# Performance work log

Hardware: AMD Instinct MI355X
Metric: run time of the kernel (lower is better)

The kernel has to match this reference:

```python
import jax, jax.numpy as jnp
import numpy as np

G, D, F, B, T = 8, 20, 160, 64, 2000  # groups, dims(hidden), feature=G*D, batch, time


def _lstm_layer(x, Wih, Whh, bih, bhh):
    # x: [B, T, Din]; Wih: [4H, Din]; Whh: [4H, H]; PyTorch gate order i,f,g,o
    H = Whh.shape[1]
    xw = jnp.einsum('btd,gd->btg', x, Wih) + bih + bhh  # [B, T, 4H]
    xw = jnp.swapaxes(xw, 0, 1)  # [T, B, 4H]
    h0 = jnp.zeros((x.shape[0], H), x.dtype)

    def step(carry, xw_t):
        h, c = carry
        gates = xw_t + h @ Whh.T
        i, f, g, o = jnp.split(gates, 4, axis=-1)
        c = jax.nn.sigmoid(f) * c + jax.nn.sigmoid(i) * jnp.tanh(g)
        h = jax.nn.sigmoid(o) * jnp.tanh(c)
        return (h, c), h

    _, hs = jax.lax.scan(step, (h0, h0), xw)
    return jnp.swapaxes(hs, 0, 1)  # [B, T, H]


def _lstm2(xg, Wih0, Whh0, bih0, bhh0, Wih1, Whh1, bih1, bhh1):
    h = _lstm_layer(xg, Wih0, Whh0, bih0, bhh0)
    return _lstm_layer(h, Wih1, Whh1, bih1, bhh1)


_run_groups = jax.vmap(_lstm2)  # map over leading group axis of inputs and params


def setup_inputs() -> dict:
    key = jax.random.key(0)
    ks = jax.random.split(key, 14)
    s = 1.0 / np.sqrt(D)
    inp = {
        'x': jax.random.normal(ks[0], (B, T, G, D), jnp.float32),
        'W_ih0': jax.random.uniform(ks[1], (G, 4 * D, D), jnp.float32, -s, s),
        'W_hh0': jax.random.uniform(ks[2], (G, 4 * D, D), jnp.float32, -s, s),
        'b_ih0': jax.random.uniform(ks[3], (G, 4 * D), jnp.float32, -s, s),
        'b_hh0': jax.random.uniform(ks[4], (G, 4 * D), jnp.float32, -s, s),
        'W_ih1': jax.random.uniform(ks[5], (G, 4 * D, D), jnp.float32, -s, s),
        'W_hh1': jax.random.uniform(ks[6], (G, 4 * D, D), jnp.float32, -s, s),
        'b_ih1': jax.random.uniform(ks[7], (G, 4 * D), jnp.float32, -s, s),
        'b_hh1': jax.random.uniform(ks[8], (G, 4 * D), jnp.float32, -s, s),
        'W1': jax.random.uniform(ks[9], (4 * F, F), jnp.float32, -1 / np.sqrt(F), 1 / np.sqrt(F)),
        'b1': jax.random.uniform(ks[10], (4 * F,), jnp.float32, -1 / np.sqrt(F), 1 / np.sqrt(F)),
        'W2': jax.random.uniform(ks[11], (F, 4 * F), jnp.float32, -1 / np.sqrt(4 * F), 1 / np.sqrt(4 * F)),
        'b2': jax.random.uniform(ks[12], (F,), jnp.float32, -1 / np.sqrt(4 * F), 1 / np.sqrt(4 * F)),
    }
    return inp


def reference(x, W_ih0, W_hh0, b_ih0, b_hh0, W_ih1, W_hh1, b_ih1, b_hh1, W1, b1, W2, b2):
    # x: [B, T, G, D] -> per-group 2-layer LSTM -> concat bands -> residual -> MLP
    xg = jnp.transpose(x, (2, 0, 1, 3))  # [G, B, T, D]
    out = _run_groups(xg, W_ih0, W_hh0, b_ih0, b_hh0, W_ih1, W_hh1, b_ih1, b_hh1)  # [G, B, T, D]
    out = jnp.transpose(out, (1, 2, 0, 3)).reshape(x.shape[0], x.shape[1], G * D)  # [B, T, F]
    fullband = out + x.reshape(x.shape[0], x.shape[1], G * D)
    h = jax.nn.relu(fullband @ W1.T + b1)
    return h @ W2.T + b2  # [B, T, F]
```

## Files before the change

### kernel.cpp

```cpp
#include <hip/hip_runtime.h>


#define Gn 8
#define Dn 20
#define Bn 64
#define Tn 2000
#define Fn 160
#define NR (Bn * Tn)
#define L2E 1.4426950408889634f

typedef __attribute__((ext_vector_type(2))) float f32x2;
typedef __attribute__((ext_vector_type(4))) float f32x4;
typedef __attribute__((ext_vector_type(8))) short bf16x8;
typedef __attribute__((ext_vector_type(2))) unsigned u32x2;

__device__ __forceinline__ float rdlane(float v, int k) {
  return __int_as_float(__builtin_amdgcn_readlane(__float_as_int(v), k));
}
__device__ __forceinline__ float xswap(float v) {
#if __has_builtin(__builtin_amdgcn_permlane32_swap)
  const u32x2 r = __builtin_amdgcn_permlane32_swap(__float_as_uint(v),
                                                   __float_as_uint(v), false,
                                                   false);
  return __uint_as_float(r.y);
#else
  return __shfl_xor(v, 32);
#endif
}
__device__ __forceinline__ unsigned short f2bf(float f) {
  unsigned u = __float_as_uint(f);
  u += 0x8000u;
  return (unsigned short)(u >> 16);
}

__device__ __forceinline__ void rec2(float gzA, float gzB,
                                     const f32x2* __restrict__ WPA,
                                     const f32x2* __restrict__ WPB, float& h,
                                     float& c) {
  f32x2 hp[10];
#pragma unroll
  for (int j = 0; j < 10; ++j) {
    hp[j].x = rdlane(h, 2 * j);
    hp[j].y = rdlane(h, 2 * j + 1);
  }
  f32x2 aA;
  aA.x = gzA;
  aA.y = 0.f;
  f32x2 aB;
  aB.x = gzB;
  aB.y = 0.f;
#pragma unroll
  for (int j = 0; j < 10; ++j) {
    aA = __builtin_elementwise_fma(WPA[j], hp[j], aA);
    aB = __builtin_elementwise_fma(WPB[j], hp[j], aB);
  }
  const float zA = aA.x + aA.y;
  const float zB = aB.x + aB.y;
  const float rA = __builtin_amdgcn_rcpf(1.f + __builtin_amdgcn_exp2f(zA));
  const float rB = __builtin_amdgcn_rcpf(1.f + __builtin_amdgcn_exp2f(zB));
  const float sF = xswap(rA);
  const float sO = xswap(rB);
  const float tG = __builtin_fmaf(-2.f, rB, 1.f);
  c = sF * c + rA * tG;
  const float tC = __builtin_fmaf(
      -2.f, __builtin_amdgcn_rcpf(1.f + __builtin_amdgcn_exp2f((2.f * L2E) * c)),
      1.f);
  h = sO * tC;
}

__device__ __forceinline__ void proj2(const float* __restrict__ row,
                                      const f32x2* __restrict__ WPA,
                                      const f32x2* __restrict__ WPB, float bzA,
                                      float bzB, float* dA, float* dB) {
  const f32x4 x0 = *(const f32x4*)&row[0];
  const f32x4 x1 = *(const f32x4*)&row[4];
  const f32x4 x2 = *(const f32x4*)&row[8];
  const f32x4 x3 = *(const f32x4*)&row[12];
  const f32x4 x4 = *(const f32x4*)&row[16];
  f32x2 xp[10];
  xp[0] = __builtin_shufflevector(x0, x0, 0, 1);
  xp[1] = __builtin_shufflevector(x0, x0, 2, 3);
  xp[2] = __builtin_shufflevector(x1, x1, 0, 1);
  xp[3] = __builtin_shufflevector(x1, x1, 2, 3);
  xp[4] = __builtin_shufflevector(x2, x2, 0, 1);
  xp[5] = __builtin_shufflevector(x2, x2, 2, 3);
  xp[6] = __builtin_shufflevector(x3, x3, 0, 1);
  xp[7] = __builtin_shufflevector(x3, x3, 2, 3);
  xp[8] = __builtin_shufflevector(x4, x4, 0, 1);
  xp[9] = __builtin_shufflevector(x4, x4, 2, 3);
  f32x2 aA;
  aA.x = bzA;
  aA.y = 0.f;
  f32x2 aB;
  aB.x = bzB;
  aB.y = 0.f;
#pragma unroll
  for (int j = 0; j < 10; ++j) {
    aA = __builtin_elementwise_fma(WPA[j], xp[j], aA);
    aB = __builtin_elementwise_fma(WPB[j], xp[j], aB);
  }
  *dA = aA.x + aA.y;
  *dB = aB.x + aB.y;
}

__global__ __launch_bounds__(512) void scan4p_kernel(
    const float* __restrict__ x, const float* __restrict__ Wih0,
    const float* __restrict__ Whh0, const float* __restrict__ bih0,
    const float* __restrict__ bhh0, const float* __restrict__ Wih1,
    const float* __restrict__ Whh1, const float* __restrict__ bih1,
    const float* __restrict__ bhh1, float* __restrict__ out) {
  __shared__ __align__(16) float XS[2][64][20];
  __shared__ __align__(16) float XW0[2][16][128];
  __shared__ __align__(16) float XW1[2][16][128];
  __shared__ __align__(16) float H0[2][16][20];

  const int tid = threadIdx.x;
  const int lane = tid & 63;
  const int wv = tid >> 6;
  const int sub = wv >> 2;
  const int wr = wv & 3;
  const int role = sub ? (3 - wr) : wr;
  const int chain = blockIdx.x * 2 + sub;
  const int g = chain >> 6;
  const int b = chain & 63;

  float (*const xs)[20] = XS[sub];
  float (*const xw0)[128] = XW0[sub];
  float (*const xw1)[128] = XW1[sub];
  float (*const h0r)[20] = H0[sub];

  const bool wl = lane < Dn;

  int rowA, rowB;
  float sAc, sBc;
  if (lane < 20) {
    rowA = lane; rowB = lane + 40; sAc = -L2E; sBc = 2.f * L2E;
  } else if (lane >= 32 && lane < 52) {
    rowA = lane - 12; rowB = lane + 28; sAc = -L2E; sBc = -L2E;
  } else {
    rowA = 0; rowB = 0; sAc = 0.f; sBc = 0.f;
  }

  f32x2 WPA[10], WPB[10];
  float bzA = 0.f, bzB = 0.f;
  {
    const float* Wsrc;
    const float* bi = nullptr;
    const float* bh = nullptr;
    if (role == 0) {
      Wsrc = Wih0; bi = bih0; bh = bhh0;
    } else if (role == 1) {
      Wsrc = Whh0;
    } else if (role == 2) {
      Wsrc = Wih1; bi = bih1; bh = bhh1;
    } else {
      Wsrc = Whh1;
    }
    const float* Wg = Wsrc + g * 1600;
#pragma unroll
    for (int j = 0; j < 10; ++j) {
      WPA[j].x = Wg[rowA * 20 + 2 * j] * sAc;
      WPA[j].y = Wg[rowA * 20 + 2 * j + 1] * sAc;
      WPB[j].x = Wg[rowB * 20 + 2 * j] * sBc;
      WPB[j].y = Wg[rowB * 20 + 2 * j + 1] * sBc;
    }
    if (bi) {
      bzA = (bi[g * 80 + rowA] + bh[g * 80 + rowA]) * sAc;
      bzB = (bi[g * 80 + rowB] + bh[g * 80 + rowB]) * sBc;
    }
  }

  if (role & 1) __builtin_amdgcn_s_setprio(1);

  const long long cbase = (long long)b * (Tn * Fn) + g * Dn;

  int st_t[3], st_d[3];
  bool st_v[3];
#pragma unroll
  for (int i = 0; i < 3; ++i) {
    const int idx = lane + 64 * i;
    st_v[i] = idx < 160;
    st_t[i] = idx / 20;
    st_d[i] = idx % 20;
  }

  if (role == 0) {
#pragma unroll
    for (int i = 0; i < 3; ++i)
      if (st_v[i])
        xs[st_t[i]][st_d[i]] = x[cbase + (long long)st_t[i] * Fn + st_d[i]];
  }
  __syncthreads();

  float h = 0.f, c = 0.f;

  for (int cix = 0; cix <= 252; ++cix) {
    if (role == 0) {
      const int cs = cix + 1;
      const bool dostage = (cs <= 249);
      float sv[3];
      if (dostage) {
#pragma unroll
        for (int i = 0; i < 3; ++i)
          if (st_v[i])
            sv[i] = x[cbase + (long long)(cs * 8 + st_t[i]) * Fn + st_d[i]];
      }
      if (cix <= 249) {
        const float* xsp = &xs[(cix * 8) & 63][0];
        float* xwp = &xw0[(cix * 8) & 15][0];
#pragma unroll
        for (int p = 0; p < 8; ++p)
          proj2(&xsp[p * 20], WPA, WPB, bzA, bzB, &xwp[p * 128 + lane],
                &xwp[p * 128 + 64 + lane]);
      }
      if (dostage) {
        float* xsw = &xs[(cs * 8) & 63][0];
#pragma unroll
        for (int i = 0; i < 3; ++i)
          if (st_v[i]) xsw[st_t[i] * 20 + st_d[i]] = sv[i];
      }
    } else if (role == 1) {
      if (cix >= 1 && cix <= 250) {
        const float* xwp = &xw0[((cix - 1) * 8) & 15][0];
        float* hrw = &h0r[((cix - 1) * 8) & 15][0];
        float gzA[8], gzB[8];
#pragma unroll
        for (int p = 0; p < 8; ++p) {
          gzA[p] = xwp[p * 128 + lane];
          gzB[p] = xwp[p * 128 + 64 + lane];
        }
#pragma unroll
        for (int p = 0; p < 8; ++p) {
          rec2(gzA[p], gzB[p], WPA, WPB, h, c);
          if (wl) hrw[p * 20 + lane] = h;
        }
      }
    } else if (role == 2) {
      if (cix >= 2 && cix <= 251) {
        const float* hrp = &h0r[((cix - 2) * 8) & 15][0];
        float* xwp = &xw1[((cix - 2) * 8) & 15][0];
#pragma unroll
        for (int p = 0; p < 8; ++p)
          proj2(&hrp[p * 20], WPA, WPB, bzA, bzB, &xwp[p * 128 + lane],
                &xwp[p * 128 + 64 + lane]);
      }
    } else {
      if (cix >= 3) {
        const int c8 = (cix - 3) * 8;
        const int rl = wl ? lane : 0;
        const float* xwp = &xw1[c8 & 15][0];
        const float* xsp = &xs[c8 & 63][0];
        float gzA[8], gzB[8], xr[8];
#pragma unroll
        for (int p = 0; p < 8; ++p) {
          gzA[p] = xwp[p * 128 + lane];
          gzB[p] = xwp[p * 128 + 64 + lane];
          xr[p] = xsp[p * 20 + rl];
        }
#pragma unroll
        for (int p = 0; p < 8; ++p) {
          rec2(gzA[p], gzB[p], WPA, WPB, h, c);
          if (wl) out[cbase + (long long)(c8 + p) * Fn + lane] = h + xr[p];
        }
      }
    }
    __syncthreads();
  }
}

__global__ __launch_bounds__(256) void mlp_mfma_kernel(
    float* io, const float* __restrict__ W1, const float* __restrict__ b1,
    const float* __restrict__ W2, const float* __restrict__ b2) {
  __shared__ short Ab[64 * 168];
  __shared__ short Wb[64 * 168];
  __shared__ short Hb[64 * 72];
  __shared__ short W2b[160 * 72];
  const int tid = threadIdx.x;
  const int lane = tid & 63;
  const int wv = tid >> 6;
  const long long r0 = (long long)blockIdx.x * 64;

#pragma unroll
  for (int i = 0; i < 10; ++i) {
    const int idx = tid + i * 256;
    const int r = idx / 40, kq = idx % 40;
    const float4 v = *(const float4*)(io + (r0 + r) * Fn + kq * 4);
    *(ushort4*)&Ab[r * 168 + kq * 4] =
        make_ushort4(f2bf(v.x), f2bf(v.y), f2bf(v.z), f2bf(v.w));
  }
  __syncthreads();

  const int cl = lane & 15;
  const int q8 = (lane >> 4) * 8;
  const int ar = wv * 16 + cl;
  bf16x8 afr[5];
#pragma unroll
  for (int kk = 0; kk < 5; ++kk)
    afr[kk] = *(const bf16x8*)&Ab[ar * 168 + kk * 32 + q8];

  f32x4 acc[10];
#pragma unroll
  for (int n = 0; n < 10; ++n) acc[n] = (f32x4){0.f, 0.f, 0.f, 0.f};

  for (int nc = 0; nc < 10; ++nc) {
    if (nc) __syncthreads();
#pragma unroll
    for (int i = 0; i < 10; ++i) {
      const int idx = tid + i * 256;
      const int r = idx / 40, kq = idx % 40;
      const float4 v = *(const float4*)(W1 + (nc * 64 + r) * Fn + kq * 4);
      *(ushort4*)&Wb[r * 168 + kq * 4] =
          make_ushort4(f2bf(v.x), f2bf(v.y), f2bf(v.z), f2bf(v.w));
    }
#pragma unroll
    for (int i = 0; i < 10; ++i) {
      const int idx = tid + i * 256;
      const int n = idx >> 4, kq = idx & 15;
      const float4 v = *(const float4*)(W2 + n * 640 + nc * 64 + kq * 4);
      *(ushort4*)&W2b[n * 72 + kq * 4] =
          make_ushort4(f2bf(v.x), f2bf(v.y), f2bf(v.z), f2bf(v.w));
    }
    __syncthreads();
#pragma unroll
    for (int n16 = 0; n16 < 4; ++n16) {
      f32x4 hcc = (f32x4){0.f, 0.f, 0.f, 0.f};
      const int br = n16 * 16 + cl;
#pragma unroll
      for (int kk = 0; kk < 5; ++kk) {
        const bf16x8 bfr = *(const bf16x8*)&Wb[br * 168 + kk * 32 + q8];
        hcc = __builtin_amdgcn_mfma_f32_16x16x32_bf16(afr[kk], bfr, hcc, 0, 0, 0);
      }
      const float b1v = b1[nc * 64 + n16 * 16 + cl];
      const int hrow0 = wv * 16 + (lane >> 4) * 4;
      const int hcol = n16 * 16 + cl;
#pragma unroll
      for (int r = 0; r < 4; ++r)
        Hb[(hrow0 + r) * 72 + hcol] = f2bf(fmaxf(hcc[r] + b1v, 0.f));
    }
    bf16x8 a2[2];
#pragma unroll
    for (int kk = 0; kk < 2; ++kk)
      a2[kk] = *(const bf16x8*)&Hb[ar * 72 + kk * 32 + q8];
#pragma unroll
    for (int n16 = 0; n16 < 10; ++n16) {
      const int br = n16 * 16 + cl;
#pragma unroll
      for (int kk = 0; kk < 2; ++kk) {
        const bf16x8 b2f = *(const bf16x8*)&W2b[br * 72 + kk * 32 + q8];
        acc[n16] = __builtin_amdgcn_mfma_f32_16x16x32_bf16(a2[kk], b2f, acc[n16], 0, 0, 0);
      }
    }
  }
  const int orow0 = wv * 16 + (lane >> 4) * 4;
#pragma unroll
  for (int n16 = 0; n16 < 10; ++n16) {
    const float b2v = b2[n16 * 16 + cl];
#pragma unroll
    for (int r = 0; r < 4; ++r)
      io[(r0 + orow0 + r) * Fn + n16 * 16 + cl] = acc[n16][r] + b2v;
  }
}

extern "C" void kernel_launch(void* const* d_in, const int* in_sizes, int n_in,
                              void* d_out, int out_size, void* d_ws, size_t ws_size,
                              hipStream_t stream) {
  const float* x    = (const float*)d_in[0];
  const float* Wih0 = (const float*)d_in[1];
  const float* Whh0 = (const float*)d_in[2];
  const float* bih0 = (const float*)d_in[3];
  const float* bhh0 = (const float*)d_in[4];
  const float* Wih1 = (const float*)d_in[5];
  const float* Whh1 = (const float*)d_in[6];
  const float* bih1 = (const float*)d_in[7];
  const float* bhh1 = (const float*)d_in[8];
  const float* W1   = (const float*)d_in[9];
  const float* b1   = (const float*)d_in[10];
  const float* W2   = (const float*)d_in[11];
  const float* b2   = (const float*)d_in[12];
  float* out = (float*)d_out;
  (void)d_ws; (void)ws_size;

  scan4p_kernel<<<dim3(256), dim3(512), 0, stream>>>(
      x, Wih0, Whh0, bih0, bhh0, Wih1, Whh1, bih1, bhh1, out);
  mlp_mfma_kernel<<<dim3(NR / 64), dim3(256), 0, stream>>>(out, W1, b1, W2, b2);
}
```

Measured before the change: 711.8 us.

## Pre-convert MLP weights to bf16 in workspace and split FMA accumulator chains

Adds a small prep kernel that converts W1 and W2 to bf16 once per call into the workspace. A new MLP kernel then loads these bf16 weights directly instead of converting fp32 weights in every block, which cuts global weight traffic and conversion work per tile. The LSTM recurrence and projection dot products now use two independent accumulator chains to shorten the serial FMA dependency on the critical recurrent path. The change adds an extra kernel launch and depends on workspace being available, with a fallback to the old MLP path otherwise.

```diff
diff --git a/kernel.cpp b/kernel.cpp
--- a/kernel.cpp
+++ b/kernel.cpp
@@ -8,6 +8,9 @@
 #define Fn 160
 #define NR (Bn * Tn)
 #define L2E 1.4426950408889634f
+#define WS_W1 0
+#define WS_W2 102400
+#define WS_NEED (204800 * sizeof(unsigned short))
 
 typedef __attribute__((ext_vector_type(2))) float f32x2;
 typedef __attribute__((ext_vector_type(4))) float f32x4;
@@ -43,19 +46,20 @@
     hp[j].x = rdlane(h, 2 * j);
     hp[j].y = rdlane(h, 2 * j + 1);
   }
-  f32x2 aA;
-  aA.x = gzA;
-  aA.y = 0.f;
-  f32x2 aB;
-  aB.x = gzB;
-  aB.y = 0.f;
-#pragma unroll
-  for (int j = 0; j < 10; ++j) {
-    aA = __builtin_elementwise_fma(WPA[j], hp[j], aA);
-    aB = __builtin_elementwise_fma(WPB[j], hp[j], aB);
-  }
-  const float zA = aA.x + aA.y;
-  const float zB = aB.x + aB.y;
+  f32x2 aA0, aA1, aB0, aB1;
+  aA0.x = gzA; aA0.y = 0.f;
+  aA1.x = 0.f; aA1.y = 0.f;
+  aB0.x = gzB; aB0.y = 0.f;
+  aB1.x = 0.f; aB1.y = 0.f;
+#pragma unroll
+  for (int j = 0; j < 10; j += 2) {
+    aA0 = __builtin_elementwise_fma(WPA[j], hp[j], aA0);
+    aA1 = __builtin_elementwise_fma(WPA[j + 1], hp[j + 1], aA1);
+    aB0 = __builtin_elementwise_fma(WPB[j], hp[j], aB0);
+    aB1 = __builtin_elementwise_fma(WPB[j + 1], hp[j + 1], aB1);
+  }
+  const float zA = (aA0.x + aA0.y) + (aA1.x + aA1.y);
+  const float zB = (aB0.x + aB0.y) + (aB1.x + aB1.y);
   const float rA = __builtin_amdgcn_rcpf(1.f + __builtin_amdgcn_exp2f(zA));
   const float rB = __builtin_amdgcn_rcpf(1.f + __builtin_amdgcn_exp2f(zB));
   const float sF = xswap(rA);
@@ -88,19 +92,20 @@
   xp[7] = __builtin_shufflevector(x3, x3, 2, 3);
   xp[8] = __builtin_shufflevector(x4, x4, 0, 1);
   xp[9] = __builtin_shufflevector(x4, x4, 2, 3);
-  f32x2 aA;
-  aA.x = bzA;
-  aA.y = 0.f;
-  f32x2 aB;
-  aB.x = bzB;
-  aB.y = 0.f;
-#pragma unroll
-  for (int j = 0; j < 10; ++j) {
-    aA = __builtin_elementwise_fma(WPA[j], xp[j], aA);
-    aB = __builtin_elementwise_fma(WPB[j], xp[j], aB);
-  }
-  *dA = aA.x + aA.y;
-  *dB = aB.x + aB.y;
+  f32x2 aA0, aA1, aB0, aB1;
+  aA0.x = bzA; aA0.y = 0.f;
+  aA1.x = 0.f; aA1.y = 0.f;
+  aB0.x = bzB; aB0.y = 0.f;
+  aB1.x = 0.f; aB1.y = 0.f;
+#pragma unroll
+  for (int j = 0; j < 10; j += 2) {
+    aA0 = __builtin_elementwise_fma(WPA[j], xp[j], aA0);
+    aA1 = __builtin_elementwise_fma(WPA[j + 1], xp[j + 1], aA1);
+    aB0 = __builtin_elementwise_fma(WPB[j], xp[j], aB0);
+    aB1 = __builtin_elementwise_fma(WPB[j + 1], xp[j + 1], aB1);
+  }
+  *dA = (aA0.x + aA0.y) + (aA1.x + aA1.y);
+  *dB = (aB0.x + aB0.y) + (aB1.x + aB1.y);
 }
 
 __global__ __launch_bounds__(512) void scan4p_kernel(
@@ -265,6 +270,109 @@
       }
     }
     __syncthreads();
+  }
+}
+
+__global__ __launch_bounds__(256) void wprep_kernel(
+    const float* __restrict__ W1, const float* __restrict__ W2,
+    unsigned short* __restrict__ wb) {
+  const int t = blockIdx.x * 256 + threadIdx.x;
+  const float4 v = (t < 25600) ? *(const float4*)(W1 + t * 4)
+                               : *(const float4*)(W2 + (t - 25600) * 4);
+  *(ushort4*)(wb + t * 4) =
+      make_ushort4(f2bf(v.x), f2bf(v.y), f2bf(v.z), f2bf(v.w));
+}
+
+__global__ __launch_bounds__(256) void mlp_bf16w_kernel(
+    float* io, const unsigned short* __restrict__ wb,
+    const float* __restrict__ b1, const float* __restrict__ b2) {
+  __shared__ short Ab[64 * 168];
+  __shared__ short Wb[64 * 168];
+  __shared__ short Hb[64 * 72];
+  __shared__ short W2b[160 * 72];
+  const unsigned short* __restrict__ W1b = wb + WS_W1;
+  const unsigned short* __restrict__ W2s = wb + WS_W2;
+  const int tid = threadIdx.x;
+  const int lane = tid & 63;
+  const int wv = tid >> 6;
+  const long long r0 = (long long)blockIdx.x * 64;
+
+#pragma unroll
+  for (int i = 0; i < 10; ++i) {
+    const int idx = tid + i * 256;
+    const int r = idx / 40, kq = idx % 40;
+    const float4 v = *(const float4*)(io + (r0 + r) * Fn + kq * 4);
+    *(ushort4*)&Ab[r * 168 + kq * 4] =
+        make_ushort4(f2bf(v.x), f2bf(v.y), f2bf(v.z), f2bf(v.w));
+  }
+  __syncthreads();
+
+  const int cl = lane & 15;
+  const int q8 = (lane >> 4) * 8;
+  const int ar = wv * 16 + cl;
+  bf16x8 afr[5];
+#pragma unroll
+  for (int kk = 0; kk < 5; ++kk)
+    afr[kk] = *(const bf16x8*)&Ab[ar * 168 + kk * 32 + q8];
+
+  f32x4 acc[10];
+#pragma unroll
+  for (int n = 0; n < 10; ++n) acc[n] = (f32x4){0.f, 0.f, 0.f, 0.f};
+
+  for (int nc = 0; nc < 10; ++nc) {
+    if (nc) __syncthreads();
+#pragma unroll
+    for (int i = 0; i < 10; ++i) {
+      const int idx = tid + i * 256;
+      const int r = idx / 40, kq = idx % 40;
+      *(ushort4*)&Wb[r * 168 + kq * 4] =
+          *(const ushort4*)(W1b + (nc * 64 + r) * 160 + kq * 4);
+    }
+#pragma unroll
+    for (int i = 0; i < 10; ++i) {
+      const int idx = tid + i * 256;
+      const int n = idx >> 4, kq = idx & 15;
+      *(ushort4*)&W2b[n * 72 + kq * 4] =
+          *(const ushort4*)(W2s + n * 640 + nc * 64 + kq * 4);
+    }
+    __syncthreads();
+#pragma unroll
+    for (int n16 = 0; n16 < 4; ++n16) {
+      f32x4 hcc = (f32x4){0.f, 0.f, 0.f, 0.f};
+      const int br = n16 * 16 + cl;
+#pragma unroll
+      for (int kk = 0; kk < 5; ++kk) {
+        const bf16x8 bfr = *(const bf16x8*)&Wb[br * 168 + kk * 32 + q8];
+        hcc = __builtin_amdgcn_mfma_f32_16x16x32_bf16(afr[kk], bfr, hcc, 0, 0, 0);
+      }
+      const float b1v = b1[nc * 64 + n16 * 16 + cl];
+      const int hrow0 = wv * 16 + (lane >> 4) * 4;
+      const int hcol = n16 * 16 + cl;
+#pragma unroll
+      for (int r = 0; r < 4; ++r)
+        Hb[(hrow0 + r) * 72 + hcol] = f2bf(fmaxf(hcc[r] + b1v, 0.f));
+    }
+    bf16x8 a2[2];
+#pragma unroll
+    for (int kk = 0; kk < 2; ++kk)
+      a2[kk] = *(const bf16x8*)&Hb[ar * 72 + kk * 32 + q8];
+#pragma unroll
+    for (int n16 = 0; n16 < 10; ++n16) {
+      const int br = n16 * 16 + cl;
+#pragma unroll
+      for (int kk = 0; kk < 2; ++kk) {
+        const bf16x8 b2f = *(const bf16x8*)&W2b[br * 72 + kk * 32 + q8];
+        acc[n16] = __builtin_amdgcn_mfma_f32_16x16x32_bf16(a2[kk], b2f, acc[n16], 0, 0, 0);
+      }
+    }
+  }
+  const int orow0 = wv * 16 + (lane >> 4) * 4;
+#pragma unroll
+  for (int n16 = 0; n16 < 10; ++n16) {
+    const float b2v = b2[n16 * 16 + cl];
+#pragma unroll
+    for (int r = 0; r < 4; ++r)
+      io[(r0 + orow0 + r) * Fn + n16 * 16 + cl] = acc[n16][r] + b2v;
   }
 }
 
@@ -378,9 +486,18 @@
   const float* W2   = (const float*)d_in[11];
   const float* b2   = (const float*)d_in[12];
   float* out = (float*)d_out;
-  (void)d_ws; (void)ws_size;
+
+  const bool fast = (d_ws != nullptr) && (ws_size >= WS_NEED);
+  if (fast)
+    wprep_kernel<<<dim3(200), dim3(256), 0, stream>>>(
+        W1, W2, (unsigned short*)d_ws);
 
   scan4p_kernel<<<dim3(256), dim3(512), 0, stream>>>(
       x, Wih0, Whh0, bih0, bhh0, Wih1, Whh1, bih1, bhh1, out);
-  mlp_mfma_kernel<<<dim3(NR / 64), dim3(256), 0, stream>>>(out, W1, b1, W2, b2);
-}
+
+  if (fast)
+    mlp_bf16w_kernel<<<dim3(NR / 64), dim3(256), 0, stream>>>(
+        out, (const unsigned short*)d_ws, b1, b2);
+  else
+    mlp_mfma_kernel<<<dim3(NR / 64), dim3(256), 0, stream>>>(out, W1, b1, W2, b2);
+}
```

New measurement: 729.6 us. +2.5%, slower.
